# Kernel optimization log

Measured on AMD Instinct MI355X. Metric: run time of the kernel, lower is better.

## Reference

```python
import jax, jax.numpy as jnp
import numpy as np

FP8_MAX = 448.0  # torch.finfo(float8_e4m3fn).max
TINY = float(np.finfo(np.float32).tiny)
BN = BK = 128  # block sizes


def _make_fp8_weight(key, N, K):
    """Mirror _create_fp8_weight: per-128x128-block scales, fp8 quantized values."""
    w = jax.random.normal(key, (N, K), jnp.float32) * 0.01
    wb = w.reshape(N // BN, BN, K // BK, BK)
    amax = jnp.abs(wb).max(axis=(1, 3))
    scale_inv = jnp.maximum(amax / FP8_MAX, TINY)  # [N/BN, K/BK]
    wq = (wb / scale_inv[:, None, :, None]).reshape(N, K)
    wq = wq.astype(jnp.float8_e4m3fn).astype(jnp.float32)  # fp8-rounded values
    return wq, scale_inv


def _dequant(wq, scale_inv):
    N, K = wq.shape
    nb, kb = scale_inv.shape
    wb = wq.reshape(nb, N // nb, kb, K // kb) * scale_inv[:, None, :, None]
    return wb.reshape(N, K)


def setup_inputs() -> dict:
    key = jax.random.key(0)
    kx, k1, k2, k3 = jax.random.split(key, 4)
    T, H, F = 4096, 2048, 7168  # tokens, hidden_dim, ffn_dim
    x = jax.random.normal(kx, (T, H), jnp.float32)
    w1_q, w1_s = _make_fp8_weight(k1, F, H)
    w3_q, w3_s = _make_fp8_weight(k3, F, H)
    w2_q, w2_s = _make_fp8_weight(k2, H, F)
    return {"hidden_states": x, "w1_q": w1_q, "w1_s": w1_s,
            "w3_q": w3_q, "w3_s": w3_s, "w2_q": w2_q, "w2_s": w2_s}


def reference(hidden_states, w1_q, w1_s, w3_q, w3_s, w2_q, w2_s):
    x = hidden_states
    w1 = _dequant(w1_q, w1_s)  # [F, H]
    w3 = _dequant(w3_q, w3_s)  # [F, H]
    w2 = _dequant(w2_q, w2_s)  # [H, F]
    g = x @ w1.T               # [T, F]
    u = x @ w3.T               # [T, F]
    fused = jax.nn.silu(g) * u
    return fused @ w2.T        # [T, H]
```

## Files before the change

kernel.cpp:

```cpp
#include <hip/hip_runtime.h>
#include <stdint.h>

typedef __attribute__((ext_vector_type(8))) short short8;
typedef __attribute__((ext_vector_type(4))) float floatx4;

__device__ __forceinline__ unsigned short f2bf(float f) {
  union { float f; unsigned int u; } c; c.f = f;
  unsigned int u = c.u;
  unsigned int r = (u + 0x7fffu + ((u >> 16) & 1u)) >> 16;
  return (unsigned short)r;
}
__device__ __forceinline__ float bf2f(unsigned short h) {
  union { unsigned int u; float f; } c; c.u = ((unsigned int)h) << 16;
  return c.f;
}

__device__ __forceinline__ void load16_to_lds(const void* g, void* l) {
  __builtin_amdgcn_global_load_lds(
      (const __attribute__((address_space(1))) unsigned int*)g,
      (__attribute__((address_space(3))) unsigned int*)l, 16, 0, 0);
}

__global__ void f32_to_bf16_kernel(const float* __restrict__ in,
                                   unsigned short* __restrict__ out, long n4) {
  long i = blockIdx.x * (long)blockDim.x + threadIdx.x;
  if (i >= n4) return;
  float4 v = ((const float4*)in)[i];
  ushort4 o;
  o.x = f2bf(v.x); o.y = f2bf(v.y); o.z = f2bf(v.z); o.w = f2bf(v.w);
  ((ushort4*)out)[i] = o;
}

__global__ void dequant2_kernel(const float* __restrict__ w1q,
                                const float* __restrict__ s1,
                                const float* __restrict__ w3q,
                                const float* __restrict__ s3,
                                unsigned short* __restrict__ o1,
                                unsigned short* __restrict__ o3,
                                int K, int sK) {
  int n = blockIdx.y;
  int k = blockIdx.x * 1024 + threadIdx.x * 4;
  size_t idx = (size_t)n * K + k;
  int sidx = (n >> 7) * sK + (k >> 7);
  float sc1 = s1[sidx], sc3 = s3[sidx];
  float4 v1 = *(const float4*)(w1q + idx);
  float4 v3 = *(const float4*)(w3q + idx);
  ushort4 a, b;
  a.x = f2bf(v1.x * sc1); a.y = f2bf(v1.y * sc1);
  a.z = f2bf(v1.z * sc1); a.w = f2bf(v1.w * sc1);
  b.x = f2bf(v3.x * sc3); b.y = f2bf(v3.y * sc3);
  b.z = f2bf(v3.z * sc3); b.w = f2bf(v3.w * sc3);
  *(ushort4*)(o1 + idx) = a;
  *(ushort4*)(o3 + idx) = b;
}

__global__ void dequant1_kernel(const float* __restrict__ wq,
                                const float* __restrict__ s,
                                unsigned short* __restrict__ out,
                                int K, int sK) {
  int n = blockIdx.y;
  int k = blockIdx.x * 1024 + threadIdx.x * 4;
  size_t idx = (size_t)n * K + k;
  float sc = s[(n >> 7) * sK + (k >> 7)];
  float4 v = *(const float4*)(wq + idx);
  ushort4 o;
  o.x = f2bf(v.x * sc); o.y = f2bf(v.y * sc);
  o.z = f2bf(v.z * sc); o.w = f2bf(v.w * sc);
  *(ushort4*)(out + idx) = o;
}

__global__ __launch_bounds__(512, 4) void dual_gemm_silu(
    const unsigned short* __restrict__ A,
    const unsigned short* __restrict__ B1,
    const unsigned short* __restrict__ B3,
    unsigned short* __restrict__ C,
    int M, int N, int K) {
  __shared__ unsigned short As[128 * 32];
  __shared__ unsigned short B1s[128 * 32];
  __shared__ unsigned short B3s[128 * 32];

  const int tid = threadIdx.x;
  const int lane = tid & 63;
  const int wave = tid >> 6;
  const int wm = wave >> 2;
  const int wn = wave & 3;
  const int m0 = blockIdx.y * 128, n0 = blockIdx.x * 128;

  const int f0 = tid * 8;
  const int ar = tid >> 2;
  const int ac = (tid & 3) * 8;

  const int q = lane >> 4;
  const int r16 = lane & 15;

  floatx4 acc_g[4][2], acc_u[4][2];
#pragma unroll
  for (int i = 0; i < 4; i++)
#pragma unroll
    for (int j = 0; j < 2; j++) {
      acc_g[i][j] = (floatx4){0.f, 0.f, 0.f, 0.f};
      acc_u[i][j] = (floatx4){0.f, 0.f, 0.f, 0.f};
    }

  const unsigned short* ag = A + (size_t)(m0 + ar) * K + ac;
  const unsigned short* b1g = B1 + (size_t)(n0 + ar) * K + ac;
  const unsigned short* b3g = B3 + (size_t)(n0 + ar) * K + ac;

  for (int k0 = 0; k0 < K; k0 += 32) {
    load16_to_lds(ag + k0, &As[f0]);
    load16_to_lds(b1g + k0, &B1s[f0]);
    load16_to_lds(b3g + k0, &B3s[f0]);
    __syncthreads();

    short8 a[4], b1[2], b3[2];
#pragma unroll
    for (int t = 0; t < 4; t++)
      a[t] = *(const short8*)&As[(wm * 64 + t * 16 + r16) * 32 + q * 8];
#pragma unroll
    for (int j = 0; j < 2; j++) {
      b1[j] = *(const short8*)&B1s[(wn * 32 + j * 16 + r16) * 32 + q * 8];
      b3[j] = *(const short8*)&B3s[(wn * 32 + j * 16 + r16) * 32 + q * 8];
    }
#pragma unroll
    for (int i = 0; i < 4; i++)
#pragma unroll
      for (int j = 0; j < 2; j++) {
        acc_g[i][j] =
            __builtin_amdgcn_mfma_f32_16x16x32_bf16(a[i], b1[j], acc_g[i][j], 0, 0, 0);
        acc_u[i][j] =
            __builtin_amdgcn_mfma_f32_16x16x32_bf16(a[i], b3[j], acc_u[i][j], 0, 0, 0);
      }
    __syncthreads();
  }

#pragma unroll
  for (int i = 0; i < 4; i++) {
    int row0 = m0 + wm * 64 + i * 16 + q * 4;
#pragma unroll
    for (int j = 0; j < 2; j++) {
      int col = n0 + wn * 32 + j * 16 + r16;
#pragma unroll
      for (int rr = 0; rr < 4; rr++) {
        float gv = acc_g[i][j][rr];
        float uv = acc_u[i][j][rr];
        float sv = gv / (1.f + __expf(-gv)) * uv;
        C[(size_t)(row0 + rr) * N + col] = f2bf(sv);
      }
    }
  }
}

__global__ __launch_bounds__(512, 4) void gemm_nt_f32_8w(
    const unsigned short* __restrict__ A,
    const unsigned short* __restrict__ B,
    float* __restrict__ C,
    int M, int N, int K) {
  __shared__ unsigned short As[128 * 32];
  __shared__ unsigned short Bs[128 * 32];

  const int tid = threadIdx.x;
  const int lane = tid & 63;
  const int wave = tid >> 6;
  const int wm = wave >> 2;
  const int wn = wave & 3;
  const int m0 = blockIdx.y * 128, n0 = blockIdx.x * 128;

  const int f0 = tid * 8;
  const int ar = tid >> 2;
  const int ac = (tid & 3) * 8;

  const int q = lane >> 4;
  const int r16 = lane & 15;

  floatx4 acc[4][2];
#pragma unroll
  for (int i = 0; i < 4; i++)
#pragma unroll
    for (int j = 0; j < 2; j++) acc[i][j] = (floatx4){0.f, 0.f, 0.f, 0.f};

  const unsigned short* ag = A + (size_t)(m0 + ar) * K + ac;
  const unsigned short* bg = B + (size_t)(n0 + ar) * K + ac;

  for (int k0 = 0; k0 < K; k0 += 32) {
    load16_to_lds(ag + k0, &As[f0]);
    load16_to_lds(bg + k0, &Bs[f0]);
    __syncthreads();

    short8 a[4], b[2];
#pragma unroll
    for (int t = 0; t < 4; t++)
      a[t] = *(const short8*)&As[(wm * 64 + t * 16 + r16) * 32 + q * 8];
#pragma unroll
    for (int j = 0; j < 2; j++)
      b[j] = *(const short8*)&Bs[(wn * 32 + j * 16 + r16) * 32 + q * 8];
#pragma unroll
    for (int i = 0; i < 4; i++)
#pragma unroll
      for (int j = 0; j < 2; j++)
        acc[i][j] =
            __builtin_amdgcn_mfma_f32_16x16x32_bf16(a[i], b[j], acc[i][j], 0, 0, 0);
    __syncthreads();
  }

#pragma unroll
  for (int i = 0; i < 4; i++) {
    int row0 = m0 + wm * 64 + i * 16 + q * 4;
#pragma unroll
    for (int j = 0; j < 2; j++) {
      int col = n0 + wn * 32 + j * 16 + r16;
#pragma unroll
      for (int rr = 0; rr < 4; rr++)
        C[(size_t)(row0 + rr) * N + col] = acc[i][j][rr];
    }
  }
}

extern "C" void kernel_launch(void* const* d_in, const int* in_sizes, int n_in,
                              void* d_out, int out_size, void* d_ws, size_t ws_size,
                              hipStream_t stream) {
  const float* x = (const float*)d_in[0];
  const float* w1q = (const float*)d_in[1];
  const float* w1s = (const float*)d_in[2];
  const float* w3q = (const float*)d_in[3];
  const float* w3s = (const float*)d_in[4];
  const float* w2q = (const float*)d_in[5];
  const float* w2s = (const float*)d_in[6];

  const int T = 4096, H = 2048, F = 7168;

  char* ws = (char*)d_ws;
  unsigned short* xb  = (unsigned short*)ws;  ws += (size_t)T * H * 2;
  unsigned short* w1b = (unsigned short*)ws;  ws += (size_t)F * H * 2;
  unsigned short* w3b = (unsigned short*)ws;  ws += (size_t)F * H * 2;
  unsigned short* w2b = (unsigned short*)ws;  ws += (size_t)H * F * 2;
  unsigned short* g   = (unsigned short*)ws;  ws += (size_t)T * F * 2;

  long xn4 = (long)T * H / 4;

  f32_to_bf16_kernel<<<(xn4 + 255) / 256, 256, 0, stream>>>(x, xb, xn4);
  dequant2_kernel<<<dim3(H / 1024, F), 256, 0, stream>>>(
      w1q, w1s, w3q, w3s, w1b, w3b, H, H / 128);
  dequant1_kernel<<<dim3(F / 1024, H), 256, 0, stream>>>(
      w2q, w2s, w2b, F, F / 128);

  dual_gemm_silu<<<dim3(F / 128, T / 128), 512, 0, stream>>>(xb, w1b, w3b, g, T, F, H);

  gemm_nt_f32_8w<<<dim3(H / 128, T / 128), 512, 0, stream>>>(g, w2b, (float*)d_out, T, H, F);
}
```

Measured before the change: 648.4 us.

## Double K-tile depth to 64 and XOR-swizzle LDS layout in both GEMMs

Both GEMM kernels now stage a 64-wide K slice per iteration instead of 32, which halves the number of barrier pairs per output tile. Each thread issues two direct-to-LDS loads per operand, and the global source column is XOR-permuted by row so that the 16-byte MFMA operand reads from LDS avoid bank conflicts. This doubles LDS use per block, which may limit the four-blocks-per-CU occupancy target. It also adds some index arithmetic.

After: 573.7 us. 11.5% less time.

```diff
diff --git a/kernel.cpp b/kernel.cpp
--- a/kernel.cpp
+++ b/kernel.cpp
@@ -69,15 +69,16 @@
   *(ushort4*)(out + idx) = o;
 }
 
+
 __global__ __launch_bounds__(512, 4) void dual_gemm_silu(
     const unsigned short* __restrict__ A,
     const unsigned short* __restrict__ B1,
     const unsigned short* __restrict__ B3,
     unsigned short* __restrict__ C,
     int M, int N, int K) {
-  __shared__ unsigned short As[128 * 32];
-  __shared__ unsigned short B1s[128 * 32];
-  __shared__ unsigned short B3s[128 * 32];
+  __shared__ unsigned short As[128 * 64];
+  __shared__ unsigned short B1s[128 * 64];
+  __shared__ unsigned short B3s[128 * 64];
 
   const int tid = threadIdx.x;
   const int lane = tid & 63;
@@ -86,12 +87,13 @@
   const int wn = wave & 3;
   const int m0 = blockIdx.y * 128, n0 = blockIdx.x * 128;
 
-  const int f0 = tid * 8;
-  const int ar = tid >> 2;
-  const int ac = (tid & 3) * 8;
+  const int s0 = tid, s1 = tid + 512;
+  const int r0 = s0 >> 3, c0 = ((s0 & 7) ^ (r0 & 7)) * 8;
+  const int r1 = s1 >> 3, c1 = ((s1 & 7) ^ (r1 & 7)) * 8;
 
   const int q = lane >> 4;
   const int r16 = lane & 15;
+  const int rx = r16 & 7;
 
   floatx4 acc_g[4][2], acc_u[4][2];
 #pragma unroll
@@ -102,34 +104,48 @@
       acc_u[i][j] = (floatx4){0.f, 0.f, 0.f, 0.f};
     }
 
-  const unsigned short* ag = A + (size_t)(m0 + ar) * K + ac;
-  const unsigned short* b1g = B1 + (size_t)(n0 + ar) * K + ac;
-  const unsigned short* b3g = B3 + (size_t)(n0 + ar) * K + ac;
-
-  for (int k0 = 0; k0 < K; k0 += 32) {
-    load16_to_lds(ag + k0, &As[f0]);
-    load16_to_lds(b1g + k0, &B1s[f0]);
-    load16_to_lds(b3g + k0, &B3s[f0]);
-    __syncthreads();
-
-    short8 a[4], b1[2], b3[2];
-#pragma unroll
-    for (int t = 0; t < 4; t++)
-      a[t] = *(const short8*)&As[(wm * 64 + t * 16 + r16) * 32 + q * 8];
-#pragma unroll
-    for (int j = 0; j < 2; j++) {
-      b1[j] = *(const short8*)&B1s[(wn * 32 + j * 16 + r16) * 32 + q * 8];
-      b3[j] = *(const short8*)&B3s[(wn * 32 + j * 16 + r16) * 32 + q * 8];
-    }
-#pragma unroll
-    for (int i = 0; i < 4; i++)
+  const unsigned short* ag0 = A + (size_t)(m0 + r0) * K + c0;
+  const unsigned short* ag1 = A + (size_t)(m0 + r1) * K + c1;
+  const unsigned short* b1g0 = B1 + (size_t)(n0 + r0) * K + c0;
+  const unsigned short* b1g1 = B1 + (size_t)(n0 + r1) * K + c1;
+  const unsigned short* b3g0 = B3 + (size_t)(n0 + r0) * K + c0;
+  const unsigned short* b3g1 = B3 + (size_t)(n0 + r1) * K + c1;
+
+  for (int k0 = 0; k0 < K; k0 += 64) {
+    load16_to_lds(ag0 + k0, &As[s0 * 8]);
+    load16_to_lds(ag1 + k0, &As[s1 * 8]);
+    load16_to_lds(b1g0 + k0, &B1s[s0 * 8]);
+    load16_to_lds(b1g1 + k0, &B1s[s1 * 8]);
+    load16_to_lds(b3g0 + k0, &B3s[s0 * 8]);
+    load16_to_lds(b3g1 + k0, &B3s[s1 * 8]);
+    __syncthreads();
+
+#pragma unroll
+    for (int kh = 0; kh < 2; kh++) {
+      const int kq = kh * 4 + q;
+      short8 a[4], b1v[2], b3v[2];
+#pragma unroll
+      for (int t = 0; t < 4; t++) {
+        int row = wm * 64 + t * 16 + r16;
+        a[t] = *(const short8*)&As[(row * 8 + (kq ^ rx)) * 8];
+      }
 #pragma unroll
       for (int j = 0; j < 2; j++) {
-        acc_g[i][j] =
-            __builtin_amdgcn_mfma_f32_16x16x32_bf16(a[i], b1[j], acc_g[i][j], 0, 0, 0);
-        acc_u[i][j] =
-            __builtin_amdgcn_mfma_f32_16x16x32_bf16(a[i], b3[j], acc_u[i][j], 0, 0, 0);
-      }
+        int row = wn * 32 + j * 16 + r16;
+        int u = (row * 8 + (kq ^ rx)) * 8;
+        b1v[j] = *(const short8*)&B1s[u];
+        b3v[j] = *(const short8*)&B3s[u];
+      }
+#pragma unroll
+      for (int i = 0; i < 4; i++)
+#pragma unroll
+        for (int j = 0; j < 2; j++) {
+          acc_g[i][j] = __builtin_amdgcn_mfma_f32_16x16x32_bf16(
+              a[i], b1v[j], acc_g[i][j], 0, 0, 0);
+          acc_u[i][j] = __builtin_amdgcn_mfma_f32_16x16x32_bf16(
+              a[i], b3v[j], acc_u[i][j], 0, 0, 0);
+        }
+    }
     __syncthreads();
   }
 
@@ -155,8 +171,8 @@
     const unsigned short* __restrict__ B,
     float* __restrict__ C,
     int M, int N, int K) {
-  __shared__ unsigned short As[128 * 32];
-  __shared__ unsigned short Bs[128 * 32];
+  __shared__ unsigned short As[128 * 64];
+  __shared__ unsigned short Bs[128 * 64];
 
   const int tid = threadIdx.x;
   const int lane = tid & 63;
@@ -165,12 +181,13 @@
   const int wn = wave & 3;
   const int m0 = blockIdx.y * 128, n0 = blockIdx.x * 128;
 
-  const int f0 = tid * 8;
-  const int ar = tid >> 2;
-  const int ac = (tid & 3) * 8;
+  const int s0 = tid, s1 = tid + 512;
+  const int r0 = s0 >> 3, c0 = ((s0 & 7) ^ (r0 & 7)) * 8;
+  const int r1 = s1 >> 3, c1 = ((s1 & 7) ^ (r1 & 7)) * 8;
 
   const int q = lane >> 4;
   const int r16 = lane & 15;
+  const int rx = r16 & 7;
 
   floatx4 acc[4][2];
 #pragma unroll
@@ -178,27 +195,39 @@
 #pragma unroll
     for (int j = 0; j < 2; j++) acc[i][j] = (floatx4){0.f, 0.f, 0.f, 0.f};
 
-  const unsigned short* ag = A + (size_t)(m0 + ar) * K + ac;
-  const unsigned short* bg = B + (size_t)(n0 + ar) * K + ac;
-
-  for (int k0 = 0; k0 < K; k0 += 32) {
-    load16_to_lds(ag + k0, &As[f0]);
-    load16_to_lds(bg + k0, &Bs[f0]);
-    __syncthreads();
-
-    short8 a[4], b[2];
-#pragma unroll
-    for (int t = 0; t < 4; t++)
-      a[t] = *(const short8*)&As[(wm * 64 + t * 16 + r16) * 32 + q * 8];
-#pragma unroll
-    for (int j = 0; j < 2; j++)
-      b[j] = *(const short8*)&Bs[(wn * 32 + j * 16 + r16) * 32 + q * 8];
-#pragma unroll
-    for (int i = 0; i < 4; i++)
-#pragma unroll
-      for (int j = 0; j < 2; j++)
-        acc[i][j] =
-            __builtin_amdgcn_mfma_f32_16x16x32_bf16(a[i], b[j], acc[i][j], 0, 0, 0);
+  const unsigned short* ag0 = A + (size_t)(m0 + r0) * K + c0;
+  const unsigned short* ag1 = A + (size_t)(m0 + r1) * K + c1;
+  const unsigned short* bg0 = B + (size_t)(n0 + r0) * K + c0;
+  const unsigned short* bg1 = B + (size_t)(n0 + r1) * K + c1;
+
+  for (int k0 = 0; k0 < K; k0 += 64) {
+    load16_to_lds(ag0 + k0, &As[s0 * 8]);
+    load16_to_lds(ag1 + k0, &As[s1 * 8]);
+    load16_to_lds(bg0 + k0, &Bs[s0 * 8]);
+    load16_to_lds(bg1 + k0, &Bs[s1 * 8]);
+    __syncthreads();
+
+#pragma unroll
+    for (int kh = 0; kh < 2; kh++) {
+      const int kq = kh * 4 + q;
+      short8 a[4], b[2];
+#pragma unroll
+      for (int t = 0; t < 4; t++) {
+        int row = wm * 64 + t * 16 + r16;
+        a[t] = *(const short8*)&As[(row * 8 + (kq ^ rx)) * 8];
+      }
+#pragma unroll
+      for (int j = 0; j < 2; j++) {
+        int row = wn * 32 + j * 16 + r16;
+        b[j] = *(const short8*)&Bs[(row * 8 + (kq ^ rx)) * 8];
+      }
+#pragma unroll
+      for (int i = 0; i < 4; i++)
+#pragma unroll
+        for (int j = 0; j < 2; j++)
+          acc[i][j] = __builtin_amdgcn_mfma_f32_16x16x32_bf16(
+              a[i], b[j], acc[i][j], 0, 0, 0);
+    }
     __syncthreads();
   }
 
```
